# Kernel optimization log

Hardware: AMD Instinct MI355X
Metric: run time of the kernel (lower is better)

Reference implementation:

```python
import jax, jax.numpy as jnp
import numpy as np

CROP = 14          # initial_crop_size
POOL_K = 2         # maxpool_kernel_size == maxpool_stride


def setup_inputs() -> dict:
    key = jax.random.key(0)
    k1, k2 = jax.random.split(key)
    features = jax.random.normal(k1, (1, 50, 50, 1024), dtype=jnp.float32)
    raw = jax.random.uniform(k2, (1, 300, 4), dtype=jnp.float32)
    # well-formed normalized boxes: y1<=y2, x1<=x2
    ys = jnp.sort(raw[..., 0::2], axis=-1)
    xs = jnp.sort(raw[..., 1::2], axis=-1)
    boxes = jnp.stack([ys[..., 0], xs[..., 0], ys[..., 1], xs[..., 1]], axis=-1)
    return {"features": features, "boxes": boxes}


def _crop_and_resize(feat, boxes, crop_size):
    # feat: [H, W, C]; boxes: [N, 4] normalized (y1, x1, y2, x2)
    # Matches tf.image.crop_and_resize bilinear semantics for crop_size > 1.
    H, W, _ = feat.shape
    y1, x1, y2, x2 = boxes[:, 0], boxes[:, 1], boxes[:, 2], boxes[:, 3]
    grid = jnp.arange(crop_size, dtype=feat.dtype)  # [S]
    # sample coordinates in source pixel space: [N, S]
    ys = y1[:, None] * (H - 1) + grid[None, :] * ((y2 - y1) * (H - 1) / (crop_size - 1))[:, None]
    xs = x1[:, None] * (W - 1) + grid[None, :] * ((x2 - x1) * (W - 1) / (crop_size - 1))[:, None]
    y0f = jnp.floor(ys)
    x0f = jnp.floor(xs)
    wy = (ys - y0f)[:, :, None, None]  # [N, S, 1, 1]
    wx = (xs - x0f)[:, None, :, None]  # [N, 1, S, 1]
    y0 = jnp.clip(y0f.astype(jnp.int32), 0, H - 1)
    y1i = jnp.clip(y0 + 1, 0, H - 1)
    x0 = jnp.clip(x0f.astype(jnp.int32), 0, W - 1)
    x1i = jnp.clip(x0 + 1, 0, W - 1)
    # four corner gathers -> [N, S, S, C]
    tl = feat[y0[:, :, None], x0[:, None, :]]
    tr = feat[y0[:, :, None], x1i[:, None, :]]
    bl = feat[y1i[:, :, None], x0[:, None, :]]
    br = feat[y1i[:, :, None], x1i[:, None, :]]
    top = tl + (tr - tl) * wx
    bot = bl + (br - bl) * wx
    return top + (bot - top) * wy


def reference(features, boxes):
    # features: [1, H, W, C]; boxes: [1, N, 4]
    crops = _crop_and_resize(features[0], boxes[0], CROP)  # [N, 14, 14, C]
    N, S, _, C = crops.shape
    P = S // POOL_K
    # 2x2 stride-2 max pool (kernel == stride, S even)
    pooled = crops.reshape(N, P, POOL_K, P, POOL_K, C).max(axis=(2, 4))  # [N, 7, 7, C]
    return pooled[None]  # [1, N, 7, 7, C]
```

## Files before the change

### kernel.cpp

```cpp
#include <hip/hip_runtime.h>
#include <math.h>

#define FH 50
#define FW 50
#define FC 1024
#define NBOX 300
#define CROPSZ 14
#define PO 7

__global__ __launch_bounds__(256) void roi_pool_kernel(
    const float* __restrict__ feat,
    const float* __restrict__ boxes,
    float* __restrict__ out)
{
    const int pxy = blockIdx.x;
    const int n   = blockIdx.y;
    const int py  = pxy / PO;
    const int px  = pxy - py * PO;
    const int c4  = threadIdx.x;

    const float by1 = boxes[n * 4 + 0];
    const float bx1 = boxes[n * 4 + 1];
    const float by2 = boxes[n * 4 + 2];
    const float bx2 = boxes[n * 4 + 3];

    const float stepy = (by2 - by1) * (49.0f / 13.0f);
    const float stepx = (bx2 - bx1) * (49.0f / 13.0f);
    const float basey = by1 * 49.0f;
    const float basex = bx1 * 49.0f;

    const float4* __restrict__ f4 = reinterpret_cast<const float4*>(feat);

    float4 m;
    m.x = -INFINITY; m.y = -INFINITY; m.z = -INFINITY; m.w = -INFINITY;

    #pragma unroll
    for (int dy = 0; dy < 2; ++dy) {
        const int iy = py * 2 + dy;
        const float ys  = basey + (float)iy * stepy;
        const float y0f = floorf(ys);
        const float wy  = ys - y0f;
        int y0 = (int)y0f;
        y0 = min(max(y0, 0), FH - 1);
        const int y1i = min(y0 + 1, FH - 1);

        #pragma unroll
        for (int dx = 0; dx < 2; ++dx) {
            const int ix = px * 2 + dx;
            const float xs  = basex + (float)ix * stepx;
            const float x0f = floorf(xs);
            const float wx  = xs - x0f;
            int x0 = (int)x0f;
            x0 = min(max(x0, 0), FW - 1);
            const int x1i = min(x0 + 1, FW - 1);

            const int rT = y0  * FW;
            const int rB = y1i * FW;
            const float4 tl = f4[(rT + x0 ) * (FC / 4) + c4];
            const float4 tr = f4[(rT + x1i) * (FC / 4) + c4];
            const float4 bl = f4[(rB + x0 ) * (FC / 4) + c4];
            const float4 br = f4[(rB + x1i) * (FC / 4) + c4];

            float4 v;
            {
                const float tx = tl.x + (tr.x - tl.x) * wx;
                const float bx_ = bl.x + (br.x - bl.x) * wx;
                v.x = tx + (bx_ - tx) * wy;
            }
            {
                const float ty = tl.y + (tr.y - tl.y) * wx;
                const float by_ = bl.y + (br.y - bl.y) * wx;
                v.y = ty + (by_ - ty) * wy;
            }
            {
                const float tz = tl.z + (tr.z - tl.z) * wx;
                const float bz_ = bl.z + (br.z - bl.z) * wx;
                v.z = tz + (bz_ - tz) * wy;
            }
            {
                const float tw = tl.w + (tr.w - tl.w) * wx;
                const float bw_ = bl.w + (br.w - bl.w) * wx;
                v.w = tw + (bw_ - tw) * wy;
            }

            m.x = fmaxf(m.x, v.x);
            m.y = fmaxf(m.y, v.y);
            m.z = fmaxf(m.z, v.z);
            m.w = fmaxf(m.w, v.w);
        }
    }

    float4* __restrict__ o4 = reinterpret_cast<float4*>(out);
    o4[(n * (PO * PO) + pxy) * (FC / 4) + c4] = m;
}

extern "C" void kernel_launch(void* const* d_in, const int* in_sizes, int n_in,
                              void* d_out, int out_size, void* d_ws, size_t ws_size,
                              hipStream_t stream) {
    const float* feat  = (const float*)d_in[0];
    const float* boxes = (const float*)d_in[1];
    float* out = (float*)d_out;

    dim3 grid(PO * PO, NBOX);
    dim3 block(256);
    roi_pool_kernel<<<grid, block, 0, stream>>>(feat, boxes, out);
}
```

Before: 119.9 us.

## Process whole pooled rows per block with sliding-window corner reuse

After: 109.7 us. 8.5% less time.

```diff
diff --git a/kernel.cpp b/kernel.cpp
--- a/kernel.cpp
+++ b/kernel.cpp
@@ -3,21 +3,35 @@
 
 #define FH 50
 #define FW 50
-#define FC 1024
+#define FC4 256
 #define NBOX 300
-#define CROPSZ 14
 #define PO 7
+
+typedef float nat4 __attribute__((ext_vector_type(4)));
+
+__device__ __forceinline__ nat4 lerp4(nat4 a, nat4 b, float w) {
+    return a + (b - a) * w;
+}
+__device__ __forceinline__ nat4 max4(nat4 a, nat4 b) {
+    nat4 r;
+    r.x = fmaxf(a.x, b.x);
+    r.y = fmaxf(a.y, b.y);
+    r.z = fmaxf(a.z, b.z);
+    r.w = fmaxf(a.w, b.w);
+    return r;
+}
 
 __global__ __launch_bounds__(256) void roi_pool_kernel(
     const float* __restrict__ feat,
     const float* __restrict__ boxes,
     float* __restrict__ out)
 {
-    const int pxy = blockIdx.x;
-    const int n   = blockIdx.y;
-    const int py  = pxy / PO;
-    const int px  = pxy - py * PO;
-    const int c4  = threadIdx.x;
+    const int j = blockIdx.x & 7;
+    const int k = blockIdx.x >> 3;
+    const int n = j + 8 * (k / PO);
+    const int py = k % PO;
+    if (n >= NBOX) return;
+    const int c4 = threadIdx.x;
 
     const float by1 = boxes[n * 4 + 0];
     const float bx1 = boxes[n * 4 + 1];
@@ -29,69 +43,61 @@
     const float basey = by1 * 49.0f;
     const float basex = bx1 * 49.0f;
 
-    const float4* __restrict__ f4 = reinterpret_cast<const float4*>(feat);
+    const float ysA = basey + (float)(2 * py) * stepy;
+    const float ysB = ysA + stepy;
+    const float fA = floorf(ysA); const float wyA = ysA - fA;
+    const float fB = floorf(ysB); const float wyB = ysB - fB;
+    int y0A = min(max((int)fA, 0), FH - 1); const int y1A = min(y0A + 1, FH - 1);
+    int y0B = min(max((int)fB, 0), FH - 1); const int y1B = min(y0B + 1, FH - 1);
 
-    float4 m;
-    m.x = -INFINITY; m.y = -INFINITY; m.z = -INFINITY; m.w = -INFINITY;
+    const nat4* __restrict__ f4 = reinterpret_cast<const nat4*>(feat);
+    const int rA0 = y0A * FW, rA1 = y1A * FW, rB0 = y0B * FW, rB1 = y1B * FW;
 
-    #pragma unroll
-    for (int dy = 0; dy < 2; ++dy) {
-        const int iy = py * 2 + dy;
-        const float ys  = basey + (float)iy * stepy;
-        const float y0f = floorf(ys);
-        const float wy  = ys - y0f;
-        int y0 = (int)y0f;
-        y0 = min(max(y0, 0), FH - 1);
-        const int y1i = min(y0 + 1, FH - 1);
+    int cc = -1000;
+    nat4 A00, A01, A10, A11, B00, B01, B10, B11;
+    A00 = A01 = A10 = A11 = B00 = B01 = B10 = B11 = (nat4)0.0f;
 
-        #pragma unroll
-        for (int dx = 0; dx < 2; ++dx) {
-            const int ix = px * 2 + dx;
-            const float xs  = basex + (float)ix * stepx;
-            const float x0f = floorf(xs);
-            const float wx  = xs - x0f;
-            int x0 = (int)x0f;
-            x0 = min(max(x0, 0), FW - 1);
-            const int x1i = min(x0 + 1, FW - 1);
+    nat4 m = (nat4)(-INFINITY);
 
-            const int rT = y0  * FW;
-            const int rB = y1i * FW;
-            const float4 tl = f4[(rT + x0 ) * (FC / 4) + c4];
-            const float4 tr = f4[(rT + x1i) * (FC / 4) + c4];
-            const float4 bl = f4[(rB + x0 ) * (FC / 4) + c4];
-            const float4 br = f4[(rB + x1i) * (FC / 4) + c4];
+    nat4* __restrict__ o4 = reinterpret_cast<nat4*>(out);
+    nat4* __restrict__ obase = o4 + (size_t)(n * (PO * PO) + py * PO) * FC4 + c4;
 
-            float4 v;
-            {
-                const float tx = tl.x + (tr.x - tl.x) * wx;
-                const float bx_ = bl.x + (br.x - bl.x) * wx;
-                v.x = tx + (bx_ - tx) * wy;
+    for (int ix = 0; ix < 2 * PO; ++ix) {
+        const float xs = basex + (float)ix * stepx;
+        const float xf = floorf(xs);
+        const float wx = xs - xf;
+        int x0 = min(max((int)xf, 0), FW - 1);
+        const int x1 = min(x0 + 1, FW - 1);
+
+        if (x0 != cc) {
+            if (x0 == cc + 1) {
+                A00 = A01; A10 = A11; B00 = B01; B10 = B11;
+                A01 = f4[(rA0 + x1) * FC4 + c4];
+                A11 = f4[(rA1 + x1) * FC4 + c4];
+                B01 = f4[(rB0 + x1) * FC4 + c4];
+                B11 = f4[(rB1 + x1) * FC4 + c4];
+            } else {
+                A00 = f4[(rA0 + x0) * FC4 + c4];
+                A01 = f4[(rA0 + x1) * FC4 + c4];
+                A10 = f4[(rA1 + x0) * FC4 + c4];
+                A11 = f4[(rA1 + x1) * FC4 + c4];
+                B00 = f4[(rB0 + x0) * FC4 + c4];
+                B01 = f4[(rB0 + x1) * FC4 + c4];
+                B10 = f4[(rB1 + x0) * FC4 + c4];
+                B11 = f4[(rB1 + x1) * FC4 + c4];
             }
-            {
-                const float ty = tl.y + (tr.y - tl.y) * wx;
-                const float by_ = bl.y + (br.y - bl.y) * wx;
-                v.y = ty + (by_ - ty) * wy;
-            }
-            {
-                const float tz = tl.z + (tr.z - tl.z) * wx;
-                const float bz_ = bl.z + (br.z - bl.z) * wx;
-                v.z = tz + (bz_ - tz) * wy;
-            }
-            {
-                const float tw = tl.w + (tr.w - tl.w) * wx;
-                const float bw_ = bl.w + (br.w - bl.w) * wx;
-                v.w = tw + (bw_ - tw) * wy;
-            }
+            cc = x0;
+        }
 
-            m.x = fmaxf(m.x, v.x);
-            m.y = fmaxf(m.y, v.y);
-            m.z = fmaxf(m.z, v.z);
-            m.w = fmaxf(m.w, v.w);
+        const nat4 vA = lerp4(lerp4(A00, A01, wx), lerp4(A10, A11, wx), wyA);
+        const nat4 vB = lerp4(lerp4(B00, B01, wx), lerp4(B10, B11, wx), wyB);
+        m = max4(m, max4(vA, vB));
+
+        if (ix & 1) {
+            __builtin_nontemporal_store(m, obase + (ix >> 1) * FC4);
+            m = (nat4)(-INFINITY);
         }
     }
-
-    float4* __restrict__ o4 = reinterpret_cast<float4*>(out);
-    o4[(n * (PO * PO) + pxy) * (FC / 4) + c4] = m;
 }
 
 extern "C" void kernel_launch(void* const* d_in, const int* in_sizes, int n_in,
@@ -101,7 +107,7 @@
     const float* boxes = (const float*)d_in[1];
     float* out = (float*)d_out;
 
-    dim3 grid(PO * PO, NBOX);
+    dim3 grid(8 * 38 * PO);
     dim3 block(256);
     roi_pool_kernel<<<grid, block, 0, stream>>>(feat, boxes, out);
 }
```
